# Kernel optimization log

Measured on AMD Instinct MI355X. Metric: run time of the kernel, lower is better.

## Reference

```python
import jax, jax.numpy as jnp
import numpy as np

DIM = 1024
N_HEADS = 16
HEAD_DIM = DIM // N_HEADS
HIDDEN = 2816
SEQ = 4096
BATCH = 1
NORM_EPS = 1e-5


def setup_inputs() -> dict:
    key = jax.random.key(0)
    ks = jax.random.split(key, 9)
    s = 1.0 / np.sqrt(DIM)
    return {
        "x": jax.random.normal(ks[0], (BATCH, SEQ, DIM), jnp.float32),
        "wq": jax.random.normal(ks[1], (DIM, DIM), jnp.float32) * s,
        "wk": jax.random.normal(ks[2], (DIM, DIM), jnp.float32) * s,
        "wv": jax.random.normal(ks[3], (DIM, DIM), jnp.float32) * s,
        "wo": jax.random.normal(ks[4], (DIM, DIM), jnp.float32) * s,
        "w1": jax.random.normal(ks[5], (DIM, HIDDEN), jnp.float32) * s,
        "w2": jax.random.normal(ks[6], (HIDDEN, DIM), jnp.float32) / np.sqrt(HIDDEN),
        "w3": jax.random.normal(ks[7], (DIM, HIDDEN), jnp.float32) * s,
        "g_attn_norm": jnp.ones((DIM,), jnp.float32),
        "g_ffn_norm": jnp.ones((DIM,), jnp.float32),
    }


def rmsnorm(x, g):
    # x: [b, s, d]; compute in fp32 as in the torch module, then cast back
    xf = x.astype(jnp.float32)
    n = xf * jax.lax.rsqrt(jnp.mean(xf * xf, axis=-1, keepdims=True) + NORM_EPS)
    return n.astype(x.dtype) * g


def attention(x, wq, wk, wv, wo):
    b, s, _ = x.shape
    q = (x @ wq).reshape(b, s, N_HEADS, HEAD_DIM).transpose(0, 2, 1, 3)  # [b,h,s,hd]
    k = (x @ wk).reshape(b, s, N_HEADS, HEAD_DIM).transpose(0, 2, 1, 3)
    v = (x @ wv).reshape(b, s, N_HEADS, HEAD_DIM).transpose(0, 2, 1, 3)
    scores = jnp.einsum("bhqd,bhkd->bhqk", q, k) / np.sqrt(HEAD_DIM)
    causal = jnp.tril(jnp.ones((s, s), bool))
    scores = jnp.where(causal, scores, -jnp.inf)
    probs = jax.nn.softmax(scores.astype(jnp.float32), axis=-1).astype(q.dtype)
    out = jnp.einsum("bhqk,bhkd->bhqd", probs, v)
    out = out.transpose(0, 2, 1, 3).reshape(b, s, DIM)
    return out @ wo


def feed_forward(x, w1, w2, w3):
    return (jax.nn.silu(x @ w1) * (x @ w3)) @ w2


def reference(x, wq, wk, wv, wo, w1, w2, w3, g_attn_norm, g_ffn_norm):
    h = x + attention(rmsnorm(x, g_attn_norm), wq, wk, wv, wo)
    out = h + feed_forward(rmsnorm(h, g_ffn_norm), w1, w2, w3)
    return out
```

## Files before the change

kernel.cpp:

```cpp
#include <hip/hip_runtime.h>
#include <stdint.h>


typedef unsigned short u16;
typedef unsigned int u32;
typedef __attribute__((ext_vector_type(8))) short short8;
typedef __attribute__((ext_vector_type(4))) float f32x4;

#define GLD16(G, L) __builtin_amdgcn_global_load_lds( \
    (__attribute__((address_space(1))) void*)(G),      \
    (__attribute__((address_space(3))) void*)(L), 16, 0, 0)

__device__ __forceinline__ u16 f2bf(float f) {
  u32 u = __builtin_bit_cast(u32, f);
  u32 r = u + 0x7fffu + ((u >> 16) & 1u);
  return (u16)(r >> 16);
}
__device__ __forceinline__ float bf2f(u16 b) {
  u32 u = (u32)b << 16;
  return __builtin_bit_cast(float, u);
}
__device__ __forceinline__ u32 pk_bf16(float lo, float hi) {
  u32 r;
  asm("v_cvt_pk_bf16_f32 %0, %1, %2" : "=v"(r) : "v"(lo), "v"(hi));
  return r;
}

__global__ __launch_bounds__(256) void k_tc4(const float* __restrict__ s0,
                                             const float* __restrict__ s1,
                                             const float* __restrict__ s2,
                                             const float* __restrict__ s3,
                                             u16* __restrict__ out, int R, int C) {
  const int z = blockIdx.z;
  const float* in = (z == 0) ? s0 : (z == 1) ? s1 : (z == 2) ? s2 : s3;
  u16* o = out + (size_t)z * R * C;
  __shared__ float t[32][33];
  const int tx = threadIdx.x & 31, ty = threadIdx.x >> 5;
  const int c0 = blockIdx.x * 32, r0 = blockIdx.y * 32;
#pragma unroll
  for (int i = 0; i < 32; i += 8)
    t[ty + i][tx] = in[(size_t)(r0 + ty + i) * C + (c0 + tx)];
  __syncthreads();
#pragma unroll
  for (int i = 0; i < 32; i += 8)
    o[(size_t)(c0 + ty + i) * R + (r0 + tx)] = f2bf(t[tx][ty + i]);
}

__global__ __launch_bounds__(256) void k_rms(const float* __restrict__ x,
                                             const float* __restrict__ g,
                                             u16* __restrict__ o) {
  const int row = blockIdx.x, tid = threadIdx.x;
  const float4 v = ((const float4*)(x + (size_t)row * 1024))[tid];
  float ss = v.x * v.x + v.y * v.y + v.z * v.z + v.w * v.w;
#pragma unroll
  for (int ofs = 32; ofs > 0; ofs >>= 1) ss += __shfl_xor(ss, ofs);
  __shared__ float red[4];
  if ((tid & 63) == 0) red[tid >> 6] = ss;
  __syncthreads();
  const float s = rsqrtf((red[0] + red[1] + red[2] + red[3]) * (1.f / 1024.f) + 1e-5f);
  const float4 gv = ((const float4*)g)[tid];
  u32 lo = (u32)f2bf(v.x * s * gv.x) | ((u32)f2bf(v.y * s * gv.y) << 16);
  u32 hi = (u32)f2bf(v.z * s * gv.z) | ((u32)f2bf(v.w * s * gv.w) << 16);
  *(uint2*)(o + (size_t)row * 1024 + tid * 4) = make_uint2(lo, hi);
}

template <int EPI, int TN>
__global__ __launch_bounds__(256) void k_gemm(const u16* __restrict__ A,
                                              const u16* __restrict__ Bt,
                                              u16* __restrict__ Obf,
                                              float* __restrict__ Of,
                                              const float* __restrict__ Rz,
                                              int M, int N, int K) {
  constexpr int NFR = TN / 32;
  __shared__ __align__(16) u16 As[128 * 32];
  __shared__ __align__(16) u16 Bs[TN * 32];
  const int tid = threadIdx.x;
  const int lane = tid & 63, wave = tid >> 6;
  const int wr = wave >> 1, wc = wave & 1;
  const int li = lane & 15, lg = lane >> 4;
  const int row0 = blockIdx.y * 128, col0 = blockIdx.x * TN;

  f32x4 acc[4][NFR] = {};
  const int sr = tid >> 2, sc = (tid & 3) * 8;
  const u16* ag = A + (size_t)(row0 + sr) * K + sc;
  const u16* bg = Bt + (size_t)(col0 + sr) * K + sc;
  u16* al = As + tid * 8;
  u16* bl = Bs + tid * 8;
  const size_t rstep = (size_t)64 * K;

  for (int k0 = 0; k0 < K; k0 += 32) {
    __syncthreads();
    GLD16(ag + k0, al);
    GLD16(ag + rstep + k0, al + 2048);
    GLD16(bg + k0, bl);
    if constexpr (TN == 128) GLD16(bg + rstep + k0, bl + 2048);
    __syncthreads();
    short8 af[4], bfr[NFR];
#pragma unroll
    for (int m = 0; m < 4; ++m)
      af[m] = *(const short8*)(As + (wr * 64 + m * 16 + li) * 32 + lg * 8);
#pragma unroll
    for (int n = 0; n < NFR; ++n)
      bfr[n] = *(const short8*)(Bs + (wc * (TN / 2) + n * 16 + li) * 32 + lg * 8);
#pragma unroll
    for (int m = 0; m < 4; ++m)
#pragma unroll
      for (int n = 0; n < NFR; ++n)
        acc[m][n] = __builtin_amdgcn_mfma_f32_16x16x32_bf16(af[m], bfr[n], acc[m][n], 0, 0, 0);
  }

#pragma unroll
  for (int m = 0; m < 4; ++m) {
    const int row = row0 + wr * 64 + m * 16 + lg * 4;
#pragma unroll
    for (int n = 0; n < NFR; ++n) {
      const int col = col0 + wc * (TN / 2) + n * 16 + li;
#pragma unroll
      for (int r = 0; r < 4; ++r) {
        const size_t idx = (size_t)(row + r) * N + col;
        if (EPI == 0) Obf[idx] = f2bf(acc[m][n][r]);
        else          Of[idx] = acc[m][n][r] + Rz[idx];
      }
    }
  }
}

__global__ __launch_bounds__(256) void k_ffn13(const u16* __restrict__ A,
                                               const u16* __restrict__ B1,
                                               const u16* __restrict__ B3,
                                               u16* __restrict__ O,
                                               int M, int N, int K) {
  __shared__ __align__(16) u16 As[128 * 32];
  __shared__ __align__(16) u16 B1s[64 * 32];
  __shared__ __align__(16) u16 B3s[64 * 32];
  const int tid = threadIdx.x;
  const int lane = tid & 63, wave = tid >> 6;
  const int wr = wave >> 1, wc = wave & 1;
  const int li = lane & 15, lg = lane >> 4;
  const int row0 = blockIdx.y * 128, col0 = blockIdx.x * 64;

  f32x4 a1[4][2] = {}, a3[4][2] = {};
  const int sr = tid >> 2, sc = (tid & 3) * 8;
  const u16* ag = A + (size_t)(row0 + sr) * K + sc;
  const u16* b1g = B1 + (size_t)(col0 + sr) * K + sc;
  const u16* b3g = B3 + (size_t)(col0 + sr) * K + sc;
  u16* al = As + tid * 8;
  u16* b1l = B1s + tid * 8;
  u16* b3l = B3s + tid * 8;
  const size_t rstep = (size_t)64 * K;

  for (int k0 = 0; k0 < K; k0 += 32) {
    __syncthreads();
    GLD16(ag + k0, al);
    GLD16(ag + rstep + k0, al + 2048);
    GLD16(b1g + k0, b1l);
    GLD16(b3g + k0, b3l);
    __syncthreads();
    short8 af[4], b1f[2], b3f[2];
#pragma unroll
    for (int m = 0; m < 4; ++m)
      af[m] = *(const short8*)(As + (wr * 64 + m * 16 + li) * 32 + lg * 8);
#pragma unroll
    for (int n = 0; n < 2; ++n) {
      b1f[n] = *(const short8*)(B1s + (wc * 32 + n * 16 + li) * 32 + lg * 8);
      b3f[n] = *(const short8*)(B3s + (wc * 32 + n * 16 + li) * 32 + lg * 8);
    }
#pragma unroll
    for (int m = 0; m < 4; ++m)
#pragma unroll
      for (int n = 0; n < 2; ++n) {
        a1[m][n] = __builtin_amdgcn_mfma_f32_16x16x32_bf16(af[m], b1f[n], a1[m][n], 0, 0, 0);
        a3[m][n] = __builtin_amdgcn_mfma_f32_16x16x32_bf16(af[m], b3f[n], a3[m][n], 0, 0, 0);
      }
  }

#pragma unroll
  for (int m = 0; m < 4; ++m) {
    const int row = row0 + wr * 64 + m * 16 + lg * 4;
#pragma unroll
    for (int n = 0; n < 2; ++n) {
      const int col = col0 + wc * 32 + n * 16 + li;
#pragma unroll
      for (int r = 0; r < 4; ++r) {
        const float g1 = a1[m][n][r], g3 = a3[m][n][r];
        const float sl = g1 / (1.f + __expf(-g1));
        O[(size_t)(row + r) * N + col] = f2bf(sl * g3);
      }
    }
  }
}

__global__ __launch_bounds__(512) void k_attn(const u16* __restrict__ qkv,
                                              u16* __restrict__ Opart,
                                              float* __restrict__ ml) {
  const int LD = 3072;
  const int b = blockIdx.x;
  const int h = b & 15;
  const int p = (b >> 4) >> 1;
  const int j = (b >> 4) & 1;
  const int tid = threadIdx.x, lane = tid & 63, w = tid >> 6;
  const int li = lane & 15, lg = lane >> 4;
  const int swzB = (li & 7) << 4;
  const float QS = 0.125f * 1.44269504f;
  const float FM = 12.0f;

  __shared__ __align__(16) u16 Ks[64 * 64];
  __shared__ __align__(16) u16 Vt[64 * 64];
  __shared__ __align__(16) u16 Ps[8 * 16 * 64];

  const int krow = tid >> 3;
  const u16* kg = qkv + 1024 + h * 64 + ((tid & 7) ^ (krow & 7)) * 8;
  u16* klds = Ks + tid * 8;

  const int vd0 = (tid & 31) * 2;
  const int vkq = tid >> 5;
  const u16* vg = qkv + 2048 + h * 64 + vd0;
  u16* vl0 = Vt + (size_t)vd0 * 64 + (((vkq * 8) ^ ((vd0 & 7) << 4)) >> 1);
  u16* vl1 = Vt + (size_t)(vd0 + 1) * 64 + (((vkq * 8) ^ (((vd0 + 1) & 7) << 4)) >> 1);
  u16* pw = Ps + w * 1024 + li * 64;

  for (int sub = 0; sub < 2; ++sub) {
    const int qb = sub ? (31 - p) : p;
    const int q0 = qb * 128;
    const int t0 = j ? (qb + 1) : 0;
    const int t1 = j ? (2 * qb + 2) : (qb + 1);
    const int qrow = q0 + w * 16 + li;
    const int wqmax = q0 + w * 16 + 15;

    const u16* qp = qkv + (size_t)qrow * LD + h * 64;
    short8 qf0, qf1;
#pragma unroll
    for (int jj = 0; jj < 8; ++jj) {
      qf0[jj] = (short)f2bf(bf2f(qp[lg * 8 + jj]) * QS);
      qf1[jj] = (short)f2bf(bf2f(qp[32 + lg * 8 + jj]) * QS);
    }

    float lsm = 0.f;
    f32x4 accO[4] = {};
    u32 vld[4];
#pragma unroll
    for (int i = 0; i < 4; ++i)
      vld[i] = *(const u32*)(vg + (size_t)(t0 * 64 + vkq * 4 + i) * LD);

    for (int t = t0; t < t1; ++t) {
      const int k0 = t * 64;
      __syncthreads();
      GLD16(kg + (size_t)(k0 + krow) * LD, klds);
      {
        u32 lo0 = (vld[0] & 0xffffu) | (vld[1] << 16);
        u32 lo1 = (vld[2] & 0xffffu) | (vld[3] << 16);
        u32 hi0 = (vld[0] >> 16) | (vld[1] & 0xffff0000u);
        u32 hi1 = (vld[2] >> 16) | (vld[3] & 0xffff0000u);
        *(uint2*)vl0 = make_uint2(lo0, lo1);
        *(uint2*)vl1 = make_uint2(hi0, hi1);
      }
      __syncthreads();
      if (t + 1 < t1) {
        const u16* vp = vg + (size_t)(t + 1) * 64 * LD;
#pragma unroll
        for (int i = 0; i < 4; ++i) vld[i] = *(const u32*)(vp + (size_t)(vkq * 4 + i) * LD);
      }

      if (k0 <= wqmax) {
        f32x4 st[4];
#pragma unroll
        for (int f = 0; f < 4; ++f) {
          const u16* kp = Ks + (size_t)(f * 16 + li) * 64;
          const short8 ka0 = *(const short8*)(kp + (((lg * 16) ^ swzB) >> 1));
          const short8 ka1 = *(const short8*)(kp + (((64 + lg * 16) ^ swzB) >> 1));
          f32x4 z = {-FM, -FM, -FM, -FM};
          z = __builtin_amdgcn_mfma_f32_16x16x32_bf16(ka0, qf0, z, 0, 0, 0);
          st[f] = __builtin_amdgcn_mfma_f32_16x16x32_bf16(ka1, qf1, z, 0, 0, 0);
        }
        if (!(k0 + 63 <= q0 + w * 16)) {
#pragma unroll
          for (int f = 0; f < 4; ++f)
#pragma unroll
            for (int r = 0; r < 4; ++r) {
              const int kg2 = k0 + f * 16 + lg * 4 + r;
              if (kg2 > qrow) st[f][r] = -1e30f;
            }
        }
        float psum = 0.f;
#pragma unroll
        for (int f = 0; f < 4; ++f) {
          const float p0 = __builtin_amdgcn_exp2f(st[f][0]);
          const float p1 = __builtin_amdgcn_exp2f(st[f][1]);
          const float p2 = __builtin_amdgcn_exp2f(st[f][2]);
          const float p3 = __builtin_amdgcn_exp2f(st[f][3]);
          psum += (p0 + p1) + (p2 + p3);
          *(uint2*)(pw + (((f * 32 + lg * 8) ^ swzB) >> 1)) =
              make_uint2(pk_bf16(p0, p1), pk_bf16(p2, p3));
        }
        psum += __shfl_xor(psum, 16);
        psum += __shfl_xor(psum, 32);
        lsm += psum;

#pragma unroll
        for (int kk = 0; kk < 2; ++kk) {
          const int cofs = ((kk * 64 + lg * 16) ^ swzB) >> 1;
          const short8 pf = *(const short8*)(pw + cofs);
#pragma unroll
          for (int n = 0; n < 4; ++n) {
            const short8 vf = *(const short8*)(Vt + (size_t)(n * 16 + li) * 64 + cofs);
            accO[n] = __builtin_amdgcn_mfma_f32_16x16x32_bf16(vf, pf, accO[n], 0, 0, 0);
          }
        }
      }
    }

    const int item = (h * 32 + qb) * 2 + j;
    u16* op = Opart + (size_t)item * 8192 + (w * 16 + li) * 64 + lg * 4;
#pragma unroll
    for (int n = 0; n < 4; ++n)
      *(uint2*)(op + n * 16) = make_uint2(pk_bf16(accO[n][0], accO[n][1]),
                                          pk_bf16(accO[n][2], accO[n][3]));
    if (lg == 0) ml[item * 128 + w * 16 + li] = lsm;
  }
}

__global__ __launch_bounds__(256) void k_amerge(const u16* __restrict__ Opart,
                                                const float* __restrict__ ml,
                                                u16* __restrict__ o) {
  const int b = blockIdx.x;
  const int h = b & 15, qb = b >> 4;
  const int q = threadIdx.x >> 1;
  const int dh = (threadIdx.x & 1) * 32;
  const int i0 = (h * 32 + qb) * 2;
  const float l0 = ml[i0 * 128 + q];
  const float l1 = ml[(i0 + 1) * 128 + q];
  const float r = 1.f / (l0 + l1);
  const u16* p0 = Opart + (size_t)i0 * 8192 + q * 64 + dh;
  const u16* p1 = p0 + 8192;
  u16* op = o + (size_t)(qb * 128 + q) * 1024 + h * 64 + dh;
#pragma unroll
  for (int dd = 0; dd < 32; dd += 4) {
    const uint2 a = *(const uint2*)(p0 + dd);
    const uint2 c = *(const uint2*)(p1 + dd);
    const float s0 = bf2f((u16)a.x) + bf2f((u16)c.x);
    const float s1 = bf2f((u16)(a.x >> 16)) + bf2f((u16)(c.x >> 16));
    const float s2 = bf2f((u16)a.y) + bf2f((u16)c.y);
    const float s3 = bf2f((u16)(a.y >> 16)) + bf2f((u16)(c.y >> 16));
    *(uint2*)(op + dd) = make_uint2(pk_bf16(s0 * r, s1 * r), pk_bf16(s2 * r, s3 * r));
  }
}

extern "C" void kernel_launch(void* const* d_in, const int* in_sizes, int n_in,
                              void* d_out, int out_size, void* d_ws, size_t ws_size,
                              hipStream_t stream) {
  const float* x  = (const float*)d_in[0];
  const float* wq = (const float*)d_in[1];
  const float* wk = (const float*)d_in[2];
  const float* wv = (const float*)d_in[3];
  const float* wo = (const float*)d_in[4];
  const float* w1 = (const float*)d_in[5];
  const float* w2 = (const float*)d_in[6];
  const float* w3 = (const float*)d_in[7];
  const float* ga = (const float*)d_in[8];
  const float* gf = (const float*)d_in[9];
  float* out = (float*)d_out;

  char* p = (char*)d_ws;
  auto take = [&](size_t n) { char* r = p; p += (n + 255) & ~(size_t)255; return r; };
  u16* wqkvo_t = (u16*)take(4ull * 1024 * 1024 * 2);
  u16* w13_t   = (u16*)take(2ull * 2816 * 1024 * 2);
  u16* w2_t    = (u16*)take(1024ull * 2816 * 2);
  u16* xn      = (u16*)take(4096ull * 1024 * 2);
  u16* qkvb    = (u16*)take(4096ull * 3072 * 2);
  u16* atn     = (u16*)take(4096ull * 1024 * 2);
  char* uni    = take(48234496);
  u16* Opart   = (u16*)uni;
  float* mlb   = (float*)(uni + 1024ull * 8192 * 2);
  float* hb    = (float*)uni;
  u16* hn      = (u16*)(uni + 4096ull * 1024 * 4);
  u16* ffb     = (u16*)(uni + 4096ull * 1024 * 6);

  u16* wqkv_t = wqkvo_t;
  u16* wo_t   = wqkvo_t + 3ull * 1024 * 1024;
  u16* w1_t   = w13_t;
  u16* w3_t   = w13_t + 2816ull * 1024;

  k_tc4<<<dim3(32, 32, 4), 256, 0, stream>>>(wq, wk, wv, wo, wqkvo_t, 1024, 1024);
  k_tc4<<<dim3(88, 32, 2), 256, 0, stream>>>(w1, w3, w1, w3, w13_t, 1024, 2816);
  k_tc4<<<dim3(32, 88, 1), 256, 0, stream>>>(w2, w2, w2, w2, w2_t, 2816, 1024);

  k_rms<<<4096, 256, 0, stream>>>(x, ga, xn);
  k_gemm<0, 128><<<dim3(24, 32), 256, 0, stream>>>(xn, wqkv_t, qkvb, nullptr, nullptr, 4096, 3072, 1024);
  k_attn<<<512, 512, 0, stream>>>(qkvb, Opart, mlb);
  k_amerge<<<512, 256, 0, stream>>>(Opart, mlb, atn);
  k_gemm<1, 64><<<dim3(16, 32), 256, 0, stream>>>(atn, wo_t, nullptr, hb, x, 4096, 1024, 1024);
  k_rms<<<4096, 256, 0, stream>>>(hb, gf, hn);
  k_ffn13<<<dim3(44, 32), 256, 0, stream>>>(hn, w1_t, w3_t, ffb, 4096, 2816, 1024);
  k_gemm<1, 64><<<dim3(16, 32), 256, 0, stream>>>(ffb, w2_t, nullptr, out, hb, 4096, 1024, 2816);
}
```

Measured before the change: 285.0 us.

## Double-buffer LDS tiles in GEMM and fused FFN kernels to overlap loads

Both the generic GEMM and the fused w1/w3 FFN kernel now hold two LDS buffers per operand. The next K-slice is prefetched with global_load_lds while MFMAs run on the current slice, and the loop uses one barrier per iteration instead of two. The aim is to hide global-memory latency behind matrix math. The cost is twice the shared memory, which may lower occupancy. Overlap also depends on the compiler not inserting full vmcnt waits before the LDS reads, and correctness relies on the prefetched loads having completed by the end-of-iteration barrier.

```diff
diff --git a/kernel.cpp b/kernel.cpp
--- a/kernel.cpp
+++ b/kernel.cpp
@@ -72,8 +72,8 @@
                                               const float* __restrict__ Rz,
                                               int M, int N, int K) {
   constexpr int NFR = TN / 32;
-  __shared__ __align__(16) u16 As[128 * 32];
-  __shared__ __align__(16) u16 Bs[TN * 32];
+  __shared__ __align__(16) u16 As[2][128 * 32];
+  __shared__ __align__(16) u16 Bs[2][TN * 32];
   const int tid = threadIdx.x;
   const int lane = tid & 63, wave = tid >> 6;
   const int wr = wave >> 1, wc = wave & 1;
@@ -84,29 +84,37 @@
   const int sr = tid >> 2, sc = (tid & 3) * 8;
   const u16* ag = A + (size_t)(row0 + sr) * K + sc;
   const u16* bg = Bt + (size_t)(col0 + sr) * K + sc;
-  u16* al = As + tid * 8;
-  u16* bl = Bs + tid * 8;
   const size_t rstep = (size_t)64 * K;
 
+  GLD16(ag, &As[0][tid * 8]);
+  GLD16(ag + rstep, &As[0][tid * 8 + 2048]);
+  GLD16(bg, &Bs[0][tid * 8]);
+  if constexpr (TN == 128) GLD16(bg + rstep, &Bs[0][tid * 8 + 2048]);
+  __syncthreads();
+
+  int cur = 0;
   for (int k0 = 0; k0 < K; k0 += 32) {
-    __syncthreads();
-    GLD16(ag + k0, al);
-    GLD16(ag + rstep + k0, al + 2048);
-    GLD16(bg + k0, bl);
-    if constexpr (TN == 128) GLD16(bg + rstep + k0, bl + 2048);
-    __syncthreads();
+    const int nxt = cur ^ 1;
+    if (k0 + 32 < K) {
+      GLD16(ag + k0 + 32, &As[nxt][tid * 8]);
+      GLD16(ag + rstep + k0 + 32, &As[nxt][tid * 8 + 2048]);
+      GLD16(bg + k0 + 32, &Bs[nxt][tid * 8]);
+      if constexpr (TN == 128) GLD16(bg + rstep + k0 + 32, &Bs[nxt][tid * 8 + 2048]);
+    }
     short8 af[4], bfr[NFR];
 #pragma unroll
     for (int m = 0; m < 4; ++m)
-      af[m] = *(const short8*)(As + (wr * 64 + m * 16 + li) * 32 + lg * 8);
+      af[m] = *(const short8*)(&As[cur][(wr * 64 + m * 16 + li) * 32 + lg * 8]);
 #pragma unroll
     for (int n = 0; n < NFR; ++n)
-      bfr[n] = *(const short8*)(Bs + (wc * (TN / 2) + n * 16 + li) * 32 + lg * 8);
+      bfr[n] = *(const short8*)(&Bs[cur][(wc * (TN / 2) + n * 16 + li) * 32 + lg * 8]);
 #pragma unroll
     for (int m = 0; m < 4; ++m)
 #pragma unroll
       for (int n = 0; n < NFR; ++n)
         acc[m][n] = __builtin_amdgcn_mfma_f32_16x16x32_bf16(af[m], bfr[n], acc[m][n], 0, 0, 0);
+    __syncthreads();
+    cur = nxt;
   }
 
 #pragma unroll
@@ -130,9 +138,9 @@
                                                const u16* __restrict__ B3,
                                                u16* __restrict__ O,
                                                int M, int N, int K) {
-  __shared__ __align__(16) u16 As[128 * 32];
-  __shared__ __align__(16) u16 B1s[64 * 32];
-  __shared__ __align__(16) u16 B3s[64 * 32];
+  __shared__ __align__(16) u16 As[2][128 * 32];
+  __shared__ __align__(16) u16 B1s[2][64 * 32];
+  __shared__ __align__(16) u16 B3s[2][64 * 32];
   const int tid = threadIdx.x;
   const int lane = tid & 63, wave = tid >> 6;
   const int wr = wave >> 1, wc = wave & 1;
@@ -144,26 +152,31 @@
   const u16* ag = A + (size_t)(row0 + sr) * K + sc;
   const u16* b1g = B1 + (size_t)(col0 + sr) * K + sc;
   const u16* b3g = B3 + (size_t)(col0 + sr) * K + sc;
-  u16* al = As + tid * 8;
-  u16* b1l = B1s + tid * 8;
-  u16* b3l = B3s + tid * 8;
   const size_t rstep = (size_t)64 * K;
 
+  GLD16(ag, &As[0][tid * 8]);
+  GLD16(ag + rstep, &As[0][tid * 8 + 2048]);
+  GLD16(b1g, &B1s[0][tid * 8]);
+  GLD16(b3g, &B3s[0][tid * 8]);
+  __syncthreads();
+
+  int cur = 0;
   for (int k0 = 0; k0 < K; k0 += 32) {
-    __syncthreads();
-    GLD16(ag + k0, al);
-    GLD16(ag + rstep + k0, al + 2048);
-    GLD16(b1g + k0, b1l);
-    GLD16(b3g + k0, b3l);
-    __syncthreads();
+    const int nxt = cur ^ 1;
+    if (k0 + 32 < K) {
+      GLD16(ag + k0 + 32, &As[nxt][tid * 8]);
+      GLD16(ag + rstep + k0 + 32, &As[nxt][tid * 8 + 2048]);
+      GLD16(b1g + k0 + 32, &B1s[nxt][tid * 8]);
+      GLD16(b3g + k0 + 32, &B3s[nxt][tid * 8]);
+    }
     short8 af[4], b1f[2], b3f[2];
 #pragma unroll
     for (int m = 0; m < 4; ++m)
-      af[m] = *(const short8*)(As + (wr * 64 + m * 16 + li) * 32 + lg * 8);
+      af[m] = *(const short8*)(&As[cur][(wr * 64 + m * 16 + li) * 32 + lg * 8]);
 #pragma unroll
     for (int n = 0; n < 2; ++n) {
-      b1f[n] = *(const short8*)(B1s + (wc * 32 + n * 16 + li) * 32 + lg * 8);
-      b3f[n] = *(const short8*)(B3s + (wc * 32 + n * 16 + li) * 32 + lg * 8);
+      b1f[n] = *(const short8*)(&B1s[cur][(wc * 32 + n * 16 + li) * 32 + lg * 8]);
+      b3f[n] = *(const short8*)(&B3s[cur][(wc * 32 + n * 16 + li) * 32 + lg * 8]);
     }
 #pragma unroll
     for (int m = 0; m < 4; ++m)
@@ -172,6 +185,8 @@
         a1[m][n] = __builtin_amdgcn_mfma_f32_16x16x32_bf16(af[m], b1f[n], a1[m][n], 0, 0, 0);
         a3[m][n] = __builtin_amdgcn_mfma_f32_16x16x32_bf16(af[m], b3f[n], a3[m][n], 0, 0, 0);
       }
+    __syncthreads();
+    cur = nxt;
   }
 
 #pragma unroll
```

Result: faster. 262.8 us (-7.8%).
